# Optimization experiments

Hardware: AMD Instinct MI355X
Metric: run time of the kernel (lower is better)

## Reference

```python
import jax, jax.numpy as jnp
import numpy as np

B, S, D_IN, D_OUT = 4, 2048, 1024, 1024

def setup_inputs() -> dict:
    key = jax.random.key(0)
    kx, kq, kk, kv = jax.random.split(key, 4)
    sc = 1.0 / np.sqrt(D_IN)
    x = jax.random.normal(kx, (B, S, D_IN), dtype=jnp.float32)
    Wq = jax.random.normal(kq, (D_IN, D_OUT), dtype=jnp.float32) * sc
    Wk = jax.random.normal(kk, (D_IN, D_OUT), dtype=jnp.float32) * sc
    Wv = jax.random.normal(kv, (D_IN, D_OUT), dtype=jnp.float32) * sc
    return {"x": x, "Wq": Wq, "Wk": Wk, "Wv": Wv}

def reference(x, Wq, Wk, Wv):
    # x: [B,S,Din]; projections to [B,S,Dout]
    q = jnp.einsum('bsd,de->bse', x, Wq)
    k = jnp.einsum('bsd,de->bse', x, Wk)
    v = jnp.einsum('bsd,de->bse', x, Wv)
    scale = 1.0 / jnp.sqrt(jnp.asarray(q.shape[-1], q.dtype))
    scores = jnp.einsum('bqe,bke->bqk', q, k) * scale  # [B,S,S]
    causal = jnp.tril(jnp.ones((scores.shape[-2], scores.shape[-1]), dtype=bool))
    scores = jnp.where(causal, scores, -jnp.inf)
    attn = jax.nn.softmax(scores, axis=-1)
    # dropout p=0.0 -> identity
    return jnp.einsum('bqk,bke->bqe', attn, v)
```

## Files before the change

kernel.cpp:

```cpp
#include <hip/hip_runtime.h>

#define SEQ 2048
#define DIM 1024

typedef __attribute__((ext_vector_type(8))) __bf16 bf16x8;
typedef __attribute__((ext_vector_type(4))) float f32x4;

typedef __attribute__((address_space(1))) unsigned char gu8_t;
typedef __attribute__((address_space(3))) unsigned char lu8_t;

__device__ __forceinline__ void async_copy16(const void* g, void* l) {
  __builtin_amdgcn_global_load_lds((gu8_t*)g, (lu8_t*)l, 16, 0, 0);
}

__device__ __forceinline__ ushort f2bf(float f) {
  union { float f; unsigned u; } v;
  v.f = f;
  unsigned r = v.u + 0x7FFFu + ((v.u >> 16) & 1u);
  return (ushort)(r >> 16);
}

__global__ void prep(const void* __restrict__ xin, const void* __restrict__ w0,
                     const void* __restrict__ w1, const void* __restrict__ w2,
                     ushort* __restrict__ xb, ushort* __restrict__ wt,
                     int* __restrict__ flag, float* __restrict__ lsum) {
  __shared__ ushort tile[64][68];
  __shared__ int redi[4];
  const int bid = blockIdx.x;
  const int t = threadIdx.x;

  const unsigned* words = (const unsigned*)xin;
  int hits = 0;
#pragma unroll
  for (int i = 0; i < 4; i++) {
    const unsigned wv = words[t * 4 + i];
    const unsigned b = (wv >> 8) & 0x7Fu;
    hits += (b >= 0x3Bu && b <= 0x42u) ? 1 : 0;
  }
#pragma unroll
  for (int o = 32; o > 0; o >>= 1) hits += __shfl_xor(hits, o, 64);
  if ((t & 63) == 0) redi[t >> 6] = hits;
  __syncthreads();
  const int bf = (redi[0] + redi[1] + redi[2] + redi[3] > 512) ? 1 : 0;

  if (bid >= 4864) {
    reinterpret_cast<float4*>(lsum)[(bid - 4864) * 256 + t] =
        make_float4(0.f, 0.f, 0.f, 0.f);
    if (bid == 4864 && t == 0) *flag = bf;
    return;
  }

  if (bid < 4096) {
    const int i = bid * 256 + t;
    if (bf) {
      reinterpret_cast<uint4*>(xb)[i] =
          reinterpret_cast<const uint4*>(xin)[i];
    } else {
      const float4* f = reinterpret_cast<const float4*>(xin);
      const float4 a = f[2 * i], b = f[2 * i + 1];
      ushort4 lo, hi;
      lo.x = f2bf(a.x); lo.y = f2bf(a.y); lo.z = f2bf(a.z); lo.w = f2bf(a.w);
      hi.x = f2bf(b.x); hi.y = f2bf(b.y); hi.z = f2bf(b.z); hi.w = f2bf(b.w);
      reinterpret_cast<ushort4*>(xb)[2 * i] = lo;
      reinterpret_cast<ushort4*>(xb)[2 * i + 1] = hi;
    }
    return;
  }

  const int rem = bid - 4096;
  const int z = rem >> 8;
  const int within = rem & 255;
  const int c0 = (within & 15) * 64, r0 = (within >> 4) * 64;
  const void* in = (z == 0) ? w0 : (z == 1) ? w1 : w2;
  ushort* op = wt + (size_t)z * 1024 * 1024;

  if (bf) {
    const ushort* ip = (const ushort*)in;
#pragma unroll
    for (int i = 0; i < 4; i++) {
      const int lin = i * 256 + t;
      const int r = lin >> 4, c4 = (lin & 15) << 2;
      const ushort4 v = *reinterpret_cast<const ushort4*>(
          ip + (size_t)(r0 + r) * 1024 + c0 + c4);
      tile[r][c4 + 0] = v.x; tile[r][c4 + 1] = v.y;
      tile[r][c4 + 2] = v.z; tile[r][c4 + 3] = v.w;
    }
  } else {
    const float* ip = (const float*)in;
#pragma unroll
    for (int i = 0; i < 4; i++) {
      const int lin = i * 256 + t;
      const int r = lin >> 4, c4 = (lin & 15) << 2;
      const float4 v = *reinterpret_cast<const float4*>(
          ip + (size_t)(r0 + r) * 1024 + c0 + c4);
      tile[r][c4 + 0] = f2bf(v.x); tile[r][c4 + 1] = f2bf(v.y);
      tile[r][c4 + 2] = f2bf(v.z); tile[r][c4 + 3] = f2bf(v.w);
    }
  }
  __syncthreads();
#pragma unroll
  for (int i = 0; i < 4; i++) {
    const int lin = i * 256 + t;
    const int c = lin >> 4, r4 = (lin & 15) << 2;
    ushort4 v;
    v.x = tile[r4 + 0][c]; v.y = tile[r4 + 1][c];
    v.z = tile[r4 + 2][c]; v.w = tile[r4 + 3][c];
    *reinterpret_cast<ushort4*>(op + (size_t)(c0 + c) * 1024 + r0 + r4) = v;
  }
}

template <int EPI, int OUTK, int CK, int SWIZ, int M, int N, int K, long AZ,
          long BZ, long CZ, long BRS>
__global__ __launch_bounds__(256, 4) void gemm_t(
    const ushort* __restrict__ A, const ushort* __restrict__ Bt,
    void* __restrict__ Cv, const int* __restrict__ flag,
    float* __restrict__ lsum, float scale0, float scale1) {
  __shared__ ushort lA[128 * 64];
  __shared__ ushort lB[128 * 64];
  __shared__ float lsh[(EPI == 2) ? 128 : 1];

  constexpr int MT = M / 128;
  const int nT = gridDim.x;
  const int id = blockIdx.y * nT + blockIdx.x;
  const int xcd = id & 7;
  const int loc = id >> 3;
  int nt, mt;
  if constexpr (SWIZ == 1) {
    const int ng = nT >> 3;
    nt = xcd * ng + loc % ng;
    mt = loc / ng;
  } else if constexpr (SWIZ == 2) {
    if (loc <= xcd) { mt = xcd; nt = loc; }
    else { mt = MT - 1 - xcd; nt = loc - xcd - 1; }
  } else if constexpr (SWIZ == 3) {
    nt = xcd;
    mt = loc;
  } else {
    nt = loc % nT;
    mt = xcd + ((loc / nT) << 3);
  }
  const int n0 = nt * 128;
  const int m0 = mt * 128;

  const int z = blockIdx.z;
  const ushort* Ab = A + (size_t)z * AZ;
  const ushort* Bb = Bt + (size_t)z * BZ;

  const int t = threadIdx.x;
  const int lane = t & 63;
  const int w = t >> 6;
  const int wm = (w >> 1) * 64;
  const int wn = (w & 1) * 64;
  const int quad = lane >> 4;
  const int l15 = lane & 15;

  if constexpr (EPI == 2) {
    if (t < 128) lsh[t] = 1.0f / lsum[(size_t)z * M + m0 + t];
  }

  f32x4 acc[4][4] = {};

  const int kEnd = CK ? ((m0 + 128 < K) ? (m0 + 128) : K) : K;

  for (int k0 = 0; k0 < kEnd; k0 += 64) {
    __syncthreads();
#pragma unroll
    for (int g0 = 0; g0 < 1024; g0 += 256) {
      const int g = g0 + t;
      const int r = g >> 3, c = (g & 7) << 3;
      async_copy16(Ab + (size_t)(m0 + r) * K + k0 + c, lA + g * 8);
    }
#pragma unroll
    for (int g0 = 0; g0 < 1024; g0 += 256) {
      const int g = g0 + t;
      const int r = g >> 3, c = (g & 7) << 3;
      async_copy16(Bb + (size_t)(n0 + r) * BRS + k0 + c, lB + g * 8);
    }
    __syncthreads();

#pragma unroll
    for (int h = 0; h < 2; h++) {
      bf16x8 af[4], bfr[4];
#pragma unroll
      for (int mi = 0; mi < 4; mi++)
        af[mi] = *(const bf16x8*)(lA + (wm + mi * 16 + l15) * 64 + h * 32 +
                                  quad * 8);
#pragma unroll
      for (int ni = 0; ni < 4; ni++)
        bfr[ni] = *(const bf16x8*)(lB + (wn + ni * 16 + l15) * 64 + h * 32 +
                                   quad * 8);
#pragma unroll
      for (int mi = 0; mi < 4; mi++)
#pragma unroll
        for (int ni = 0; ni < 4; ni++)
          acc[mi][ni] = __builtin_amdgcn_mfma_f32_16x16x32_bf16(
              af[mi], bfr[ni], acc[mi][ni], 0, 0, 0);
    }
  }

  const size_t zc = (size_t)z * CZ;

  if constexpr (EPI == 1) {
    ushort* C = (ushort*)Cv + zc;
    float* ls = lsum + (size_t)z * M;
#pragma unroll
    for (int mi = 0; mi < 4; mi++)
#pragma unroll
      for (int r = 0; r < 4; r++) {
        const int row = m0 + wm + mi * 16 + quad * 4 + r;
        float partial = 0.0f;
#pragma unroll
        for (int ni = 0; ni < 4; ni++) {
          const int col = n0 + wn + ni * 16 + l15;
          const float ev = (col <= row) ? __expf(acc[mi][ni][r]) : 0.0f;
          C[(size_t)row * N + col] = f2bf(ev);
          partial += ev;
        }
#pragma unroll
        for (int o = 1; o < 16; o <<= 1) partial += __shfl_xor(partial, o, 64);
        if (l15 == 0) atomicAdd(&ls[row], partial);
      }
    return;
  } else {
    const float scale = (z == 0) ? scale0 : scale1;
    const bool storeBf = (OUTK == 1) || (OUTK == 2 && *flag != 0);
#pragma unroll
    for (int mi = 0; mi < 4; mi++)
#pragma unroll
      for (int ni = 0; ni < 4; ni++)
#pragma unroll
        for (int r = 0; r < 4; r++) {
          const int lrow = wm + mi * 16 + quad * 4 + r;
          const int row = m0 + lrow;
          const int col = n0 + wn + ni * 16 + l15;
          const float sc = (EPI == 2) ? lsh[lrow] : scale;
          const float vv = acc[mi][ni][r] * sc;
          if (storeBf) {
            ushort* C = (ushort*)Cv + zc;
            C[(size_t)row * N + col] = f2bf(vv);
          } else {
            float* C = (float*)Cv + zc;
            C[(size_t)row * N + col] = vv;
          }
        }
  }
}

extern "C" void kernel_launch(void* const* d_in, const int* in_sizes, int n_in,
                              void* d_out, int out_size, void* d_ws,
                              size_t ws_size, hipStream_t stream) {
  char* ws = (char*)d_ws;
  const size_t MB = 1024 * 1024;
  int* flag = (int*)ws;
  ushort* wt = (ushort*)(ws + 1 * MB);
  ushort* xb = (ushort*)(ws + 7 * MB);
  ushort* q = (ushort*)(ws + 23 * MB);
  ushort* kk = (ushort*)(ws + 39 * MB);
  ushort* vt = (ushort*)(ws + 55 * MB);
  ushort* sc = (ushort*)(ws + 71 * MB);
  float* lsum = (float*)(ws + 103 * MB);
  (void)kk;

  prep<<<dim3(4872), 256, 0, stream>>>(d_in[0], d_in[1], d_in[2], d_in[3], xb,
                                       wt, flag, lsum);

  gemm_t<0, 1, 0, 0, 8192, 1024, 1024, 0L, 1024L * 1024, 8192L * 1024, 1024L>
      <<<dim3(8, 64, 2), 256, 0, stream>>>(xb, wt, (void*)q, flag, nullptr,
                                           0.03125f, 1.0f);

  gemm_t<0, 1, 0, 1, 1024, 8192, 1024, 0L, 0L, 0L, 1024L>
      <<<dim3(64, 8, 1), 256, 0, stream>>>(wt + 2 * 1024 * 1024, xb,
                                           (void*)vt, flag, nullptr, 1.0f,
                                           1.0f);

  gemm_t<1, 1, 0, 2, 2048, 2048, 1024, (long)SEQ * DIM, (long)SEQ * DIM,
         (long)SEQ * SEQ, (long)DIM>
      <<<dim3(8, 17, 4), 256, 0, stream>>>(q, kk, (void*)sc, flag, lsum, 1.0f,
                                           1.0f);

  gemm_t<2, 2, 1, 3, 2048, 1024, 2048, (long)SEQ * SEQ, 2048L,
         (long)SEQ * DIM, 8192L>
      <<<dim3(8, 16, 4), 256, 0, stream>>>(sc, vt, d_out, flag, lsum, 1.0f,
                                           1.0f);
}
```

Before: 245.8 us.

## Add 256x256-tile 8-wave GEMM kernel fusing QKV projections and triangular QK^T

```diff
diff --git a/kernel.cpp b/kernel.cpp
--- a/kernel.cpp
+++ b/kernel.cpp
@@ -106,6 +106,220 @@
     v.x = tile[r4 + 0][c]; v.y = tile[r4 + 1][c];
     v.z = tile[r4 + 2][c]; v.w = tile[r4 + 3][c];
     *reinterpret_cast<ushort4*>(op + (size_t)(c0 + c) * 1024 + r0 + r4) = v;
+  }
+}
+
+template <int EPI>
+__global__ __launch_bounds__(512, 2) void gemm8(
+    const ushort* __restrict__ P0, const ushort* __restrict__ P1,
+    void* __restrict__ Cv, float* __restrict__ lsum) {
+  __shared__ ushort sA[2][2][128 * 64];
+  __shared__ ushort sB[2][2][128 * 64];
+
+  const ushort* A;
+  const ushort* B;
+  ushort* C;
+  float* ls = nullptr;
+  int m0, n0;
+  long ldA, ldB, ldC;
+  float scale = 1.0f;
+
+  if constexpr (EPI == 0) {
+    const int id = blockIdx.x;
+    if (id < 256) {
+      const int z = id >> 7, r = id & 127;
+      m0 = (r >> 2) << 8;
+      n0 = (r & 3) << 8;
+      A = P0; ldA = 1024;
+      B = P1 + (size_t)z * 1024 * 1024; ldB = 1024;
+      C = (ushort*)Cv + (size_t)z * 8192 * 1024; ldC = 1024;
+      scale = z ? 1.0f : 0.03125f;
+    } else {
+      const int r = id - 256;
+      m0 = (r >> 5) << 8;
+      n0 = (r & 31) << 8;
+      A = P1 + 2 * 1024 * 1024; ldA = 1024;
+      B = P0; ldB = 1024;
+      C = (ushort*)Cv + (size_t)16 * 1024 * 1024; ldC = 8192;
+    }
+  } else {
+    const int id = blockIdx.x, z = blockIdx.y;
+    int mt = 0;
+    while ((mt + 1) * (mt + 2) / 2 <= id) mt++;
+    const int nt = id - mt * (mt + 1) / 2;
+    m0 = mt << 8;
+    n0 = nt << 8;
+    A = P0 + (size_t)z * SEQ * DIM; ldA = 1024;
+    B = P0 + (size_t)8192 * 1024 + (size_t)z * SEQ * DIM; ldB = 1024;
+    C = (ushort*)Cv + (size_t)z * SEQ * SEQ; ldC = 2048;
+    ls = lsum + (size_t)z * SEQ;
+  }
+  const int nT = 16;
+
+  const int tid = threadIdx.x;
+  const int lane = tid & 63;
+  const int w = tid >> 6;
+  const int quad = lane >> 4;
+  const int l15 = lane & 15;
+  const int ah = w >> 2;
+  const int wn = (w & 3) << 6;
+  const int bh = wn >> 7;
+  const int bo = wn & 64;
+
+  const ushort* aSrc[2][2];
+  const ushort* bSrc[2][2];
+#pragma unroll
+  for (int h = 0; h < 2; h++)
+#pragma unroll
+    for (int i = 0; i < 2; i++) {
+      const int g = i * 512 + tid;
+      const int rl = g >> 3;
+      const int ck = (g & 7) ^ (rl & 7);
+      aSrc[h][i] = A + (size_t)(m0 + h * 128 + rl) * ldA + ck * 8;
+      bSrc[h][i] = B + (size_t)(n0 + h * 128 + rl) * ldB + ck * 8;
+    }
+
+  auto stageA = [&](int t, int b) {
+#pragma unroll
+    for (int h = 0; h < 2; h++)
+#pragma unroll
+      for (int i = 0; i < 2; i++)
+        async_copy16(aSrc[h][i] + t * 64, &sA[b][h][(i * 512 + tid) * 8]);
+  };
+  auto stageB = [&](int t, int b) {
+#pragma unroll
+    for (int h = 0; h < 2; h++)
+#pragma unroll
+      for (int i = 0; i < 2; i++)
+        async_copy16(bSrc[h][i] + t * 64, &sB[b][h][(i * 512 + tid) * 8]);
+  };
+  auto rdA = [&](int b, int rbase, int kh) -> bf16x8 {
+    const int row = rbase + l15;
+    const int ck = ((kh << 2) | quad) ^ (row & 7);
+    return *(const bf16x8*)&sA[b][ah][row * 64 + ck * 8];
+  };
+  auto rdB = [&](int b, int rbase, int kh) -> bf16x8 {
+    const int row = rbase + l15;
+    const int ck = ((kh << 2) | quad) ^ (row & 7);
+    return *(const bf16x8*)&sB[b][bh][row * 64 + ck * 8];
+  };
+
+  f32x4 acc[8][4] = {};
+  bf16x8 aF[8], bF0[4], bF1[4];
+
+  stageA(0, 0); stageB(0, 0);
+  stageA(1, 1); stageB(1, 1);
+  asm volatile("s_waitcnt vmcnt(8)" ::: "memory");
+  __builtin_amdgcn_s_barrier();
+
+#pragma unroll 1
+  for (int t = 0; t < nT; t++) {
+    const int b = t & 1;
+
+#pragma unroll
+    for (int m = 0; m < 4; m++)
+#pragma unroll
+      for (int h = 0; h < 2; h++) aF[m * 2 + h] = rdA(b, m * 16, h);
+#pragma unroll
+    for (int n = 0; n < 2; n++)
+#pragma unroll
+      for (int h = 0; h < 2; h++) bF0[n * 2 + h] = rdB(b, bo + n * 16, h);
+    __builtin_amdgcn_s_barrier();
+    __builtin_amdgcn_s_setprio(1);
+#pragma unroll
+    for (int h = 0; h < 2; h++)
+#pragma unroll
+      for (int m = 0; m < 4; m++)
+#pragma unroll
+        for (int n = 0; n < 2; n++)
+          acc[m][n] = __builtin_amdgcn_mfma_f32_16x16x32_bf16(
+              aF[m * 2 + h], bF0[n * 2 + h], acc[m][n], 0, 0, 0);
+    __builtin_amdgcn_s_setprio(0);
+    __builtin_amdgcn_s_barrier();
+
+#pragma unroll
+    for (int n = 0; n < 2; n++)
+#pragma unroll
+      for (int h = 0; h < 2; h++)
+        bF1[n * 2 + h] = rdB(b, bo + 32 + n * 16, h);
+    __builtin_amdgcn_s_barrier();
+    __builtin_amdgcn_s_setprio(1);
+#pragma unroll
+    for (int h = 0; h < 2; h++)
+#pragma unroll
+      for (int m = 0; m < 4; m++)
+#pragma unroll
+        for (int n = 0; n < 2; n++)
+          acc[m][2 + n] = __builtin_amdgcn_mfma_f32_16x16x32_bf16(
+              aF[m * 2 + h], bF1[n * 2 + h], acc[m][2 + n], 0, 0, 0);
+    __builtin_amdgcn_s_setprio(0);
+    __builtin_amdgcn_s_barrier();
+
+#pragma unroll
+    for (int m = 0; m < 4; m++)
+#pragma unroll
+      for (int h = 0; h < 2; h++) aF[m * 2 + h] = rdA(b, 64 + m * 16, h);
+    if (t + 2 < nT) stageB(t + 2, b);
+    __builtin_amdgcn_s_barrier();
+    __builtin_amdgcn_s_setprio(1);
+#pragma unroll
+    for (int h = 0; h < 2; h++)
+#pragma unroll
+      for (int m = 0; m < 4; m++)
+#pragma unroll
+        for (int n = 0; n < 2; n++)
+          acc[4 + m][n] = __builtin_amdgcn_mfma_f32_16x16x32_bf16(
+              aF[m * 2 + h], bF0[n * 2 + h], acc[4 + m][n], 0, 0, 0);
+    __builtin_amdgcn_s_setprio(0);
+    __builtin_amdgcn_s_barrier();
+
+    if (t + 2 < nT) stageA(t + 2, b);
+    __builtin_amdgcn_s_setprio(1);
+#pragma unroll
+    for (int h = 0; h < 2; h++)
+#pragma unroll
+      for (int m = 0; m < 4; m++)
+#pragma unroll
+        for (int n = 0; n < 2; n++)
+          acc[4 + m][2 + n] = __builtin_amdgcn_mfma_f32_16x16x32_bf16(
+              aF[m * 2 + h], bF1[n * 2 + h], acc[4 + m][2 + n], 0, 0, 0);
+    __builtin_amdgcn_s_setprio(0);
+    if (t + 2 < nT)
+      asm volatile("s_waitcnt vmcnt(8)" ::: "memory");
+    else
+      asm volatile("s_waitcnt vmcnt(0)" ::: "memory");
+    __builtin_amdgcn_s_barrier();
+  }
+
+  if constexpr (EPI == 0) {
+#pragma unroll
+    for (int mi = 0; mi < 8; mi++)
+#pragma unroll
+      for (int ni = 0; ni < 4; ni++)
+#pragma unroll
+        for (int r = 0; r < 4; r++) {
+          const int row = m0 + ah * 128 + mi * 16 + quad * 4 + r;
+          const int col = n0 + wn + ni * 16 + l15;
+          C[(size_t)row * ldC + col] = f2bf(acc[mi][ni][r] * scale);
+        }
+  } else {
+#pragma unroll
+    for (int mi = 0; mi < 8; mi++)
+#pragma unroll
+      for (int r = 0; r < 4; r++) {
+        const int row = m0 + ah * 128 + mi * 16 + quad * 4 + r;
+        float partial = 0.0f;
+#pragma unroll
+        for (int ni = 0; ni < 4; ni++) {
+          const int col = n0 + wn + ni * 16 + l15;
+          const float ev = (col <= row) ? __expf(acc[mi][ni][r]) : 0.0f;
+          C[(size_t)row * ldC + col] = f2bf(ev);
+          partial += ev;
+        }
+#pragma unroll
+        for (int o = 1; o < 16; o <<= 1) partial += __shfl_xor(partial, o, 64);
+        if (l15 == 0) atomicAdd(&ls[row], partial);
+      }
   }
 }
 
@@ -255,28 +469,16 @@
   ushort* wt = (ushort*)(ws + 1 * MB);
   ushort* xb = (ushort*)(ws + 7 * MB);
   ushort* q = (ushort*)(ws + 23 * MB);
-  ushort* kk = (ushort*)(ws + 39 * MB);
   ushort* vt = (ushort*)(ws + 55 * MB);
   ushort* sc = (ushort*)(ws + 71 * MB);
   float* lsum = (float*)(ws + 103 * MB);
-  (void)kk;
 
   prep<<<dim3(4872), 256, 0, stream>>>(d_in[0], d_in[1], d_in[2], d_in[3], xb,
                                        wt, flag, lsum);
 
-  gemm_t<0, 1, 0, 0, 8192, 1024, 1024, 0L, 1024L * 1024, 8192L * 1024, 1024L>
-      <<<dim3(8, 64, 2), 256, 0, stream>>>(xb, wt, (void*)q, flag, nullptr,
-                                           0.03125f, 1.0f);
-
-  gemm_t<0, 1, 0, 1, 1024, 8192, 1024, 0L, 0L, 0L, 1024L>
-      <<<dim3(64, 8, 1), 256, 0, stream>>>(wt + 2 * 1024 * 1024, xb,
-                                           (void*)vt, flag, nullptr, 1.0f,
-                                           1.0f);
-
-  gemm_t<1, 1, 0, 2, 2048, 2048, 1024, (long)SEQ * DIM, (long)SEQ * DIM,
-         (long)SEQ * SEQ, (long)DIM>
-      <<<dim3(8, 17, 4), 256, 0, stream>>>(q, kk, (void*)sc, flag, lsum, 1.0f,
-                                           1.0f);
+  gemm8<0><<<dim3(384), 512, 0, stream>>>(xb, wt, (void*)q, nullptr);
+
+  gemm8<1><<<dim3(36, 4), 512, 0, stream>>>(q, nullptr, (void*)sc, lsum);
 
   gemm_t<2, 2, 1, 3, 2048, 1024, 2048, (long)SEQ * SEQ, 2048L,
          (long)SEQ * DIM, 8192L>
```

Result: no change. 247.3 us (+0.6%).
